# Kernel tuning notes

Measured on AMD Instinct MI355X. Metric: run time of the kernel, lower is better.

## Reference

```python
import jax, jax.numpy as jnp
import numpy as np

N_NODES = 50000
N_EDGES = 800000
N_GRAPHS = 512
D_IN = 64
D_HID = 64
D_CLS = 128
LEAKY_SLOPE = 0.01


def _glorot(key, shape):
    fan_in, fan_out = shape[0], shape[1]
    lim = jnp.sqrt(6.0 / (fan_in + fan_out)).astype(jnp.float32)
    return jax.random.uniform(key, shape, jnp.float32, -lim, lim)


def setup_inputs() -> dict:
    key = jax.random.key(0)
    ks = jax.random.split(key, 16)
    x = jax.random.normal(ks[0], (N_NODES, D_IN), jnp.float32)
    edge_index = jax.random.randint(ks[1], (2, N_EDGES), 0, N_NODES, jnp.int32)
    batch = jnp.sort(jax.random.randint(ks[2], (N_NODES,), 0, N_GRAPHS, jnp.int32))
    return {
        'x': x,
        'W0': _glorot(ks[3], (D_IN, D_HID)), 'b0': jnp.zeros((D_HID,), jnp.float32),
        'W1': _glorot(ks[4], (D_HID, D_HID)), 'b1': jnp.zeros((D_HID,), jnp.float32),
        'W2': _glorot(ks[5], (D_HID, D_HID)), 'b2': jnp.zeros((D_HID,), jnp.float32),
        'lin1_w': _glorot(ks[6], (D_HID, D_CLS)), 'lin1_b': jnp.zeros((D_CLS,), jnp.float32),
        'lin2_w': _glorot(ks[7], (D_CLS, 1)), 'lin2_b': jnp.zeros((1,), jnp.float32),
        'fc_w': _glorot(ks[8], (1, 1)), 'fc_b': jnp.zeros((1,), jnp.float32),
        'edge_index': edge_index,
        'batch': batch,
    }


def _gcn_layer(h_in, W, b, src, dst, edge_norm, deg_inv):
    # GCNConv: linear transform, then symmetric-normalized aggregation with self-loops
    h = h_in @ W                                        # [N, D]
    msgs = h[src] * edge_norm[:, None]                  # gather + scale, [E, D]
    agg = jax.ops.segment_sum(msgs, dst, num_segments=N_NODES)  # scatter-add
    return agg + deg_inv[:, None] * h + b               # self-loop term + bias


def reference(x, W0, b0, W1, b1, W2, b2, lin1_w, lin1_b, lin2_w, lin2_b, fc_w, fc_b, edge_index, batch):
    src, dst = edge_index[0], edge_index[1]
    # degrees including self-loop (A + I)
    deg = jax.ops.segment_sum(jnp.ones((N_EDGES,), jnp.float32), dst, num_segments=N_NODES) + 1.0
    deg_inv_sqrt = jax.lax.rsqrt(deg)
    deg_inv = 1.0 / deg
    edge_norm = deg_inv_sqrt[src] * deg_inv_sqrt[dst]   # [E]

    h = _gcn_layer(x, W0, b0, src, dst, edge_norm, deg_inv)
    h = _gcn_layer(h, W1, b1, src, dst, edge_norm, deg_inv)
    h = _gcn_layer(h, W2, b2, src, dst, edge_norm, deg_inv)

    # global_mean_pool over graphs
    sums = jax.ops.segment_sum(h, batch, num_segments=N_GRAPHS)          # [G, D]
    counts = jax.ops.segment_sum(jnp.ones((N_NODES,), jnp.float32), batch, num_segments=N_GRAPHS)
    pooled = sums / jnp.maximum(counts, 1.0)[:, None]

    out = pooled @ lin1_w + lin1_b      # [G, cls_hidden]
    out = out @ lin2_w + lin2_b         # [G, 1]
    out = out @ fc_w + fc_b             # [G, 1]
    return jnp.where(out >= 0, out, LEAKY_SLOPE * out)  # LeakyReLU
```

## Files before the change

kernel.cpp:

```cpp
#include <hip/hip_runtime.h>
#include <math.h>

#define N_NODES 50000
#define N_EDGES 800000
#define N_GRAPHS 512
#define D 64
#define D_CLS 128
#define BNODES 128
#define NBUK 391
#define BSTRIDE 4096
#define PART_TILE 4096

typedef _Float16 h4 __attribute__((ext_vector_type(4)));
typedef float    f4 __attribute__((ext_vector_type(4)));

static inline int cdiv(int a, int b) { return (a + b - 1) / b; }


__global__ void k_binit(int* __restrict__ btail) {
    int b = blockIdx.x * blockDim.x + threadIdx.x;
    if (b < NBUK) btail[b] = b * BSTRIDE;
}


__global__ __launch_bounds__(256) void k_part(
        const int* __restrict__ src, const int* __restrict__ dst,
        int* __restrict__ btail, int* __restrict__ ebuf) {
    __shared__ int lcnt[NBUK];
    __shared__ int lbase[NBUK];
    int t = threadIdx.x;
    for (int i = t; i < NBUK; i += 256) lcnt[i] = 0;
    __syncthreads();

    int e0 = blockIdx.x * PART_TILE + t;
    int ent[16];
    int br[16];
    #pragma unroll
    for (int k = 0; k < 16; k++) {
        int e = e0 + k * 256;
        if (e < N_EDGES) {
            int d = dst[e];
            int b = d / BNODES;
            int r = atomicAdd(&lcnt[b], 1);
            ent[k] = src[e] | ((d & (BNODES - 1)) << 16);
            br[k] = (b << 16) | r;
        } else {
            br[k] = -1;
        }
    }
    __syncthreads();
    for (int i = t; i < NBUK; i += 256) {
        int c = lcnt[i];
        lbase[i] = c ? atomicAdd(&btail[i], c) : 0;
    }
    __syncthreads();
    #pragma unroll
    for (int k = 0; k < 16; k++) {
        if (br[k] >= 0) {
            int b = br[k] >> 16, r = br[k] & 0xFFFF;
            ebuf[lbase[b] + r] = ent[k];
        }
    }
}


__global__ __launch_bounds__(256) void k_build(
        const int* __restrict__ ebuf, const int* __restrict__ btail,
        int2* __restrict__ rng, float* __restrict__ dis,
        int* __restrict__ col) {
    __shared__ int hist[BNODES];
    __shared__ int base[BNODES];
    __shared__ int cur[BNODES];
    int t = threadIdx.x;
    int b = blockIdx.x;
    int s = b * BSTRIDE;
    int e = btail[b];

    if (t < BNODES) { hist[t] = 0; cur[t] = 0; }
    __syncthreads();

    for (int i = s + t; i < e; i += 256)
        atomicAdd(&hist[(ebuf[i] >> 16) & (BNODES - 1)], 1);
    __syncthreads();

    if (t < BNODES) base[t] = hist[t];
    __syncthreads();
    for (int off = 1; off < BNODES; off <<= 1) {
        int x = 0;
        if (t < BNODES && t >= off) x = base[t - off];
        __syncthreads();
        if (t < BNODES) base[t] += x;
        __syncthreads();
    }
    if (t < BNODES) {
        int ex = base[t] - hist[t];
        base[t] = ex;
        int n = b * BNODES + t;
        if (n < N_NODES) {
            rng[n] = make_int2(s + ex, s + ex + hist[t]);
            dis[n] = rsqrtf((float)hist[t] + 1.0f);
        }
    }
    __syncthreads();

    for (int i = s + t; i < e; i += 256) {
        int v = ebuf[i];
        int d = (v >> 16) & (BNODES - 1);
        int pos = atomicAdd(&cur[d], 1);
        col[s + base[d] + pos] = v & 0xFFFF;
    }
}


#define XS_STRIDE 68

template<bool HALF_IN>
__global__ __launch_bounds__(256) void k_gemm_scale(
        const void* __restrict__ Xv, const float* __restrict__ W,
        const float* __restrict__ dis, _Float16* __restrict__ G16) {
    __shared__ float Xs[64 * XS_STRIDE];
    __shared__ float Ws[64 * 64];
    int n0 = blockIdx.x * 64;
    int t = threadIdx.x;

    {
        int base = t * 16;
        const float4* wsrc = (const float4*)(W + base);
        float4* wdst = (float4*)(Ws + base);
        wdst[0] = wsrc[0]; wdst[1] = wsrc[1]; wdst[2] = wsrc[2]; wdst[3] = wsrc[3];
    }
    {
        int row = t >> 2;
        int c0 = (t & 3) * 16;
        int grow = n0 + row;
        float* xd = Xs + row * XS_STRIDE + c0;
        if (grow < N_NODES) {
            if (HALF_IN) {
                const h4* xp = (const h4*)((const _Float16*)Xv + (size_t)grow * D + c0);
                #pragma unroll
                for (int j = 0; j < 4; j++)
                    *(f4*)(xd + j * 4) = __builtin_convertvector(xp[j], f4);
            } else {
                const float4* xp = (const float4*)((const float*)Xv + (size_t)grow * D + c0);
                float4* xd4 = (float4*)xd;
                xd4[0] = xp[0]; xd4[1] = xp[1]; xd4[2] = xp[2]; xd4[3] = xp[3];
            }
        } else {
            float4 z = {0.f, 0.f, 0.f, 0.f};
            float4* xd4 = (float4*)xd;
            xd4[0] = z; xd4[1] = z; xd4[2] = z; xd4[3] = z;
        }
    }
    __syncthreads();

    int tc = t & 15, tr = t >> 4;
    int r0 = tr * 4, c0 = tc * 4;
    float acc[4][4] = {};
    #pragma unroll 4
    for (int k = 0; k < 64; k++) {
        float4 wv = *(const float4*)&Ws[k * 64 + c0];
        #pragma unroll
        for (int i = 0; i < 4; i++) {
            float xv = Xs[(r0 + i) * XS_STRIDE + k];
            acc[i][0] = fmaf(xv, wv.x, acc[i][0]);
            acc[i][1] = fmaf(xv, wv.y, acc[i][1]);
            acc[i][2] = fmaf(xv, wv.z, acc[i][2]);
            acc[i][3] = fmaf(xv, wv.w, acc[i][3]);
        }
    }
    #pragma unroll
    for (int i = 0; i < 4; i++) {
        int grow = n0 + r0 + i;
        if (grow < N_NODES) {
            float dsc = dis[grow];
            h4 o;
            o.x = (_Float16)(acc[i][0] * dsc);
            o.y = (_Float16)(acc[i][1] * dsc);
            o.z = (_Float16)(acc[i][2] * dsc);
            o.w = (_Float16)(acc[i][3] * dsc);
            *(h4*)&G16[(size_t)grow * D + c0] = o;
        }
    }
}


__global__ __launch_bounds__(256) void k_agg(
        const _Float16* __restrict__ G16, const int2* __restrict__ rng,
        const int* __restrict__ col, const float* __restrict__ dis,
        const float* __restrict__ bias, _Float16* __restrict__ Hout) {
    int t = threadIdx.x;
    int grp = t >> 4;
    int fl4 = (t & 15) * 4;
    int n = blockIdx.x * 16 + grp;

    int2 r = rng[n];
    int s = r.x, e = r.y;
    f4 acc = __builtin_convertvector(*(const h4*)(G16 + (size_t)n * D + fl4), f4);

    for (int i = s; i < e; i += 8) {
        int i1 = i + 1, i2 = i + 2, i3 = i + 3;
        int i4 = i + 4, i5 = i + 5, i6 = i + 6, i7 = i + 7;
        int c0 = col[i];
        int c1 = col[i1 < e ? i1 : i];
        int c2 = col[i2 < e ? i2 : i];
        int c3 = col[i3 < e ? i3 : i];
        int c4 = col[i4 < e ? i4 : i];
        int c5 = col[i5 < e ? i5 : i];
        int c6 = col[i6 < e ? i6 : i];
        int c7 = col[i7 < e ? i7 : i];
        float f1 = (i1 < e) ? 1.f : 0.f;
        float f2 = (i2 < e) ? 1.f : 0.f;
        float f3 = (i3 < e) ? 1.f : 0.f;
        float f4_ = (i4 < e) ? 1.f : 0.f;
        float f5 = (i5 < e) ? 1.f : 0.f;
        float f6 = (i6 < e) ? 1.f : 0.f;
        float f7 = (i7 < e) ? 1.f : 0.f;
        f4 g0 = __builtin_convertvector(*(const h4*)(G16 + (size_t)c0 * D + fl4), f4);
        f4 g1 = __builtin_convertvector(*(const h4*)(G16 + (size_t)c1 * D + fl4), f4);
        f4 g2 = __builtin_convertvector(*(const h4*)(G16 + (size_t)c2 * D + fl4), f4);
        f4 g3 = __builtin_convertvector(*(const h4*)(G16 + (size_t)c3 * D + fl4), f4);
        f4 g4 = __builtin_convertvector(*(const h4*)(G16 + (size_t)c4 * D + fl4), f4);
        f4 g5 = __builtin_convertvector(*(const h4*)(G16 + (size_t)c5 * D + fl4), f4);
        f4 g6 = __builtin_convertvector(*(const h4*)(G16 + (size_t)c6 * D + fl4), f4);
        f4 g7 = __builtin_convertvector(*(const h4*)(G16 + (size_t)c7 * D + fl4), f4);
        acc += g0;
        acc += f1 * g1;
        acc += f2 * g2;
        acc += f3 * g3;
        acc += f4_ * g4;
        acc += f5 * g5;
        acc += f6 * g6;
        acc += f7 * g7;
    }

    float dsc = dis[n];
    f4 bv = *(const f4*)(bias + fl4);
    f4 o = dsc * acc + bv;
    h4 oh;
    oh.x = (_Float16)o.x; oh.y = (_Float16)o.y;
    oh.z = (_Float16)o.z; oh.w = (_Float16)o.w;
    *(h4*)(Hout + (size_t)n * D + fl4) = oh;
}


__device__ __forceinline__ int lower_bound_batch(const int* batch, int g) {
    int lo = 0, hi = N_NODES;
    while (lo < hi) {
        int mid = (lo + hi) >> 1;
        if (batch[mid] < g) lo = mid + 1; else hi = mid;
    }
    return lo;
}

__global__ __launch_bounds__(128) void k_poolmlp(
        const _Float16* __restrict__ H16, const int* __restrict__ batch,
        const float* __restrict__ w1, const float* __restrict__ b1,
        const float* __restrict__ w2, const float* __restrict__ b2,
        const float* __restrict__ fcw, const float* __restrict__ fcb,
        float* __restrict__ out) {
    __shared__ float ps[64];
    __shared__ float red[128];
    int g = blockIdx.x, t = threadIdx.x;
    int s = lower_bound_batch(batch, g);
    int e = lower_bound_batch(batch, g + 1);

    int f = t & 63, slot = t >> 6;
    float acc = 0.f;
    for (int r = s + slot; r < e; r += 2)
        acc += (float)H16[(size_t)r * D + f];
    red[t] = acc;
    __syncthreads();
    if (t < 64) {
        int cnt = e - s;
        ps[t] = (red[t] + red[t + 64]) / (float)(cnt > 0 ? cnt : 1);
    }
    __syncthreads();

    float a = b1[t];
    #pragma unroll
    for (int k = 0; k < 64; k++) a = fmaf(ps[k], w1[k * D_CLS + t], a);
    red[t] = a * w2[t];
    __syncthreads();
    for (int s2 = 64; s2 > 0; s2 >>= 1) {
        if (t < s2) red[t] += red[t + s2];
        __syncthreads();
    }
    if (t == 0) {
        float o = red[0] + b2[0];
        o = fmaf(o, fcw[0], fcb[0]);
        out[g] = (o >= 0.f) ? o : 0.01f * o;
    }
}


extern "C" void kernel_launch(void* const* d_in, const int* in_sizes, int n_in,
                              void* d_out, int out_size, void* d_ws, size_t ws_size,
                              hipStream_t stream) {
    const float* x   = (const float*)d_in[0];
    const float* W0  = (const float*)d_in[1];
    const float* b0  = (const float*)d_in[2];
    const float* W1  = (const float*)d_in[3];
    const float* b1  = (const float*)d_in[4];
    const float* W2  = (const float*)d_in[5];
    const float* b2  = (const float*)d_in[6];
    const float* l1w = (const float*)d_in[7];
    const float* l1b = (const float*)d_in[8];
    const float* l2w = (const float*)d_in[9];
    const float* l2b = (const float*)d_in[10];
    const float* fcw = (const float*)d_in[11];
    const float* fcb = (const float*)d_in[12];
    const int* eidx  = (const int*)d_in[13];
    const int* batch = (const int*)d_in[14];
    const int* src = eidx;
    const int* dst = eidx + N_EDGES;

    char* ws = (char*)d_ws;
    size_t off = 0;
    auto alloc = [&](size_t bytes) -> void* {
        off = (off + 255) & ~(size_t)255;
        void* p = ws + off;
        off += bytes;
        return p;
    };

    int2*  rng    = (int2*) alloc(N_NODES * sizeof(int2));
    int*   btail  = (int*)  alloc(NBUK * sizeof(int));
    int*   ebuf   = (int*)  alloc((size_t)NBUK * BSTRIDE * sizeof(int));
    int*   col    = (int*)  alloc((size_t)NBUK * BSTRIDE * sizeof(int));
    float* dis    = (float*)alloc(N_NODES * sizeof(float));
    _Float16* G16 = (_Float16*)alloc((size_t)N_NODES * D * sizeof(_Float16));
    _Float16* H1  = (_Float16*)alloc((size_t)N_NODES * D * sizeof(_Float16));
    _Float16* H2  = (_Float16*)alloc((size_t)N_NODES * D * sizeof(_Float16));

    const int nbPart = cdiv(N_EDGES, PART_TILE);

    k_binit<<<cdiv(NBUK, 256), 256, 0, stream>>>(btail);
    k_part<<<nbPart, 256, 0, stream>>>(src, dst, btail, ebuf);
    k_build<<<NBUK, 256, 0, stream>>>(ebuf, btail, rng, dis, col);

    const int nbGemm = cdiv(N_NODES, 64);
    const int nbAgg  = cdiv(N_NODES, 16);

    k_gemm_scale<false><<<nbGemm, 256, 0, stream>>>(x, W0, dis, G16);
    k_agg<<<nbAgg, 256, 0, stream>>>(G16, rng, col, dis, b0, H1);
    k_gemm_scale<true><<<nbGemm, 256, 0, stream>>>(H1, W1, dis, G16);
    k_agg<<<nbAgg, 256, 0, stream>>>(G16, rng, col, dis, b1, H2);
    k_gemm_scale<true><<<nbGemm, 256, 0, stream>>>(H2, W2, dis, G16);
    k_agg<<<nbAgg, 256, 0, stream>>>(G16, rng, col, dis, b2, H1);

    k_poolmlp<<<N_GRAPHS, 128, 0, stream>>>(H1, batch, l1w, l1b, l2w, l2b,
                                            fcw, fcb, (float*)d_out);
}
```

Baseline: 149.4 us.

## Fuse next-layer GEMM and scaling into the aggregation kernel epilogue

```diff
diff --git a/kernel.cpp b/kernel.cpp
--- a/kernel.cpp
+++ b/kernel.cpp
@@ -114,9 +114,8 @@
 
 #define XS_STRIDE 68
 
-template<bool HALF_IN>
 __global__ __launch_bounds__(256) void k_gemm_scale(
-        const void* __restrict__ Xv, const float* __restrict__ W,
+        const float* __restrict__ X, const float* __restrict__ W,
         const float* __restrict__ dis, _Float16* __restrict__ G16) {
     __shared__ float Xs[64 * XS_STRIDE];
     __shared__ float Ws[64 * 64];
@@ -133,22 +132,13 @@
         int row = t >> 2;
         int c0 = (t & 3) * 16;
         int grow = n0 + row;
-        float* xd = Xs + row * XS_STRIDE + c0;
+        float4* xd = (float4*)(Xs + row * XS_STRIDE + c0);
         if (grow < N_NODES) {
-            if (HALF_IN) {
-                const h4* xp = (const h4*)((const _Float16*)Xv + (size_t)grow * D + c0);
-                #pragma unroll
-                for (int j = 0; j < 4; j++)
-                    *(f4*)(xd + j * 4) = __builtin_convertvector(xp[j], f4);
-            } else {
-                const float4* xp = (const float4*)((const float*)Xv + (size_t)grow * D + c0);
-                float4* xd4 = (float4*)xd;
-                xd4[0] = xp[0]; xd4[1] = xp[1]; xd4[2] = xp[2]; xd4[3] = xp[3];
-            }
+            const float4* xp = (const float4*)(X + (size_t)grow * D + c0);
+            xd[0] = xp[0]; xd[1] = xp[1]; xd[2] = xp[2]; xd[3] = xp[3];
         } else {
             float4 z = {0.f, 0.f, 0.f, 0.f};
-            float4* xd4 = (float4*)xd;
-            xd4[0] = z; xd4[1] = z; xd4[2] = z; xd4[3] = z;
+            xd[0] = z; xd[1] = z; xd[2] = z; xd[3] = z;
         }
     }
     __syncthreads();
@@ -184,11 +174,22 @@
 }
 
 
-__global__ __launch_bounds__(256) void k_agg(
+template<bool FINAL>
+__global__ __launch_bounds__(256) void k_agg_fused(
         const _Float16* __restrict__ G16, const int2* __restrict__ rng,
         const int* __restrict__ col, const float* __restrict__ dis,
-        const float* __restrict__ bias, _Float16* __restrict__ Hout) {
+        const float* __restrict__ bias, const float* __restrict__ Wn,
+        _Float16* __restrict__ Gout) {
+    __shared__ float Ws[64 * 64];
     int t = threadIdx.x;
+    if (!FINAL) {
+        int base = t * 16;
+        const float4* wsrc = (const float4*)(Wn + base);
+        float4* wdst = (float4*)(Ws + base);
+        wdst[0] = wsrc[0]; wdst[1] = wsrc[1]; wdst[2] = wsrc[2]; wdst[3] = wsrc[3];
+        __syncthreads();
+    }
+
     int grp = t >> 4;
     int fl4 = (t & 15) * 4;
     int n = blockIdx.x * 16 + grp;
@@ -235,11 +236,36 @@
 
     float dsc = dis[n];
     f4 bv = *(const f4*)(bias + fl4);
-    f4 o = dsc * acc + bv;
-    h4 oh;
-    oh.x = (_Float16)o.x; oh.y = (_Float16)o.y;
-    oh.z = (_Float16)o.z; oh.w = (_Float16)o.w;
-    *(h4*)(Hout + (size_t)n * D + fl4) = oh;
+    f4 h = dsc * acc + bv;
+
+    if (FINAL) {
+        h4 oh;
+        oh.x = (_Float16)h.x; oh.y = (_Float16)h.y;
+        oh.z = (_Float16)h.z; oh.w = (_Float16)h.w;
+        *(h4*)(Gout + (size_t)n * D + fl4) = oh;
+    } else {
+        f4 out = {0.f, 0.f, 0.f, 0.f};
+        #pragma unroll
+        for (int kk = 0; kk < 16; kk++) {
+            float h0 = __shfl(h.x, kk, 16);
+            float h1 = __shfl(h.y, kk, 16);
+            float h2 = __shfl(h.z, kk, 16);
+            float h3 = __shfl(h.w, kk, 16);
+            f4 w0 = *(const f4*)&Ws[(kk * 4 + 0) * 64 + fl4];
+            f4 w1 = *(const f4*)&Ws[(kk * 4 + 1) * 64 + fl4];
+            f4 w2 = *(const f4*)&Ws[(kk * 4 + 2) * 64 + fl4];
+            f4 w3 = *(const f4*)&Ws[(kk * 4 + 3) * 64 + fl4];
+            out += h0 * w0;
+            out += h1 * w1;
+            out += h2 * w2;
+            out += h3 * w3;
+        }
+        out *= dsc;
+        h4 oh;
+        oh.x = (_Float16)out.x; oh.y = (_Float16)out.y;
+        oh.z = (_Float16)out.z; oh.w = (_Float16)out.w;
+        *(h4*)(Gout + (size_t)n * D + fl4) = oh;
+    }
 }
 
 
@@ -328,9 +354,9 @@
     int*   ebuf   = (int*)  alloc((size_t)NBUK * BSTRIDE * sizeof(int));
     int*   col    = (int*)  alloc((size_t)NBUK * BSTRIDE * sizeof(int));
     float* dis    = (float*)alloc(N_NODES * sizeof(float));
-    _Float16* G16 = (_Float16*)alloc((size_t)N_NODES * D * sizeof(_Float16));
-    _Float16* H1  = (_Float16*)alloc((size_t)N_NODES * D * sizeof(_Float16));
-    _Float16* H2  = (_Float16*)alloc((size_t)N_NODES * D * sizeof(_Float16));
+    _Float16* Ga  = (_Float16*)alloc((size_t)N_NODES * D * sizeof(_Float16));
+    _Float16* Gb  = (_Float16*)alloc((size_t)N_NODES * D * sizeof(_Float16));
+    _Float16* H   = (_Float16*)alloc((size_t)N_NODES * D * sizeof(_Float16));
 
     const int nbPart = cdiv(N_EDGES, PART_TILE);
 
@@ -341,13 +367,11 @@
     const int nbGemm = cdiv(N_NODES, 64);
     const int nbAgg  = cdiv(N_NODES, 16);
 
-    k_gemm_scale<false><<<nbGemm, 256, 0, stream>>>(x, W0, dis, G16);
-    k_agg<<<nbAgg, 256, 0, stream>>>(G16, rng, col, dis, b0, H1);
-    k_gemm_scale<true><<<nbGemm, 256, 0, stream>>>(H1, W1, dis, G16);
-    k_agg<<<nbAgg, 256, 0, stream>>>(G16, rng, col, dis, b1, H2);
-    k_gemm_scale<true><<<nbGemm, 256, 0, stream>>>(H2, W2, dis, G16);
-    k_agg<<<nbAgg, 256, 0, stream>>>(G16, rng, col, dis, b2, H1);
-
-    k_poolmlp<<<N_GRAPHS, 128, 0, stream>>>(H1, batch, l1w, l1b, l2w, l2b,
+    k_gemm_scale<<<nbGemm, 256, 0, stream>>>(x, W0, dis, Ga);
+    k_agg_fused<false><<<nbAgg, 256, 0, stream>>>(Ga, rng, col, dis, b0, W1, Gb);
+    k_agg_fused<false><<<nbAgg, 256, 0, stream>>>(Gb, rng, col, dis, b1, W2, Ga);
+    k_agg_fused<true><<<nbAgg, 256, 0, stream>>>(Ga, rng, col, dis, b2, nullptr, H);
+
+    k_poolmlp<<<N_GRAPHS, 128, 0, stream>>>(H, batch, l1w, l1b, l2w, l2b,
                                             fcw, fcb, (float*)d_out);
 }
```

New measurement: 138.2 us. -7.5%, faster.
